# Kernel optimization log

Hardware: AMD Instinct MI355X
Metric: run time of the kernel (lower is better)

The kernel has to match this reference:

```python
import jax, jax.numpy as jnp
import numpy as np

POOL = 14
NUM_ROIS = 512
H, W, C = 200, 200, 1024


def setup_inputs() -> dict:
    key = jax.random.key(0)
    k1, k2, k3, k4, k5 = jax.random.split(key, 5)
    img = jax.random.normal(k1, (1, H, W, C), dtype=jnp.float32)
    # valid boxes: x + w <= W, y + h <= H, w,h >= 8
    x = jax.random.randint(k2, (1, NUM_ROIS), 0, W // 2)
    y = jax.random.randint(k3, (1, NUM_ROIS), 0, H // 2)
    w = jax.random.randint(k4, (1, NUM_ROIS), 8, W // 2)
    h = jax.random.randint(k5, (1, NUM_ROIS), 8, H // 2)
    rois = jnp.stack([x, y, w, h], axis=-1).astype(jnp.int32)  # [1, R, 4]
    return {"img": img, "rois": rois}


def _roi_resize(fm, box):
    # fm: [H, W, C]; box: [4] int32 (x, y, w, h)
    x, y, w, h = box[0], box[1], box[2], box[3]
    # TF1 tf.image.resize_images bilinear, align_corners=False (asymmetric):
    # src = dst * (in_size / out_size), taps floored + clamped to crop extent.
    sy = jnp.arange(POOL, dtype=jnp.float32) * (h.astype(jnp.float32) / POOL)
    sx = jnp.arange(POOL, dtype=jnp.float32) * (w.astype(jnp.float32) / POOL)
    y0 = jnp.floor(sy).astype(jnp.int32)
    x0 = jnp.floor(sx).astype(jnp.int32)
    y0c = jnp.clip(y0, 0, h - 1)
    y1c = jnp.clip(y0 + 1, 0, h - 1)
    x0c = jnp.clip(x0, 0, w - 1)
    x1c = jnp.clip(x0 + 1, 0, w - 1)
    wy = (sy - y0.astype(jnp.float32))[:, None, None]  # [P,1,1]
    wx = (sx - x0.astype(jnp.float32))[None, :, None]  # [1,P,1]
    iy0, iy1 = y + y0c, y + y1c  # absolute row indices
    ix0, ix1 = x + x0c, x + x1c  # absolute col indices
    g00 = fm[iy0[:, None], ix0[None, :]]  # [P,P,C]
    g01 = fm[iy0[:, None], ix1[None, :]]
    g10 = fm[iy1[:, None], ix0[None, :]]
    g11 = fm[iy1[:, None], ix1[None, :]]
    top = g00 + (g01 - g00) * wx
    bot = g10 + (g11 - g10) * wx
    return top + (bot - top) * wy


def reference(img, rois):
    fm = img[0]  # [H, W, C]
    out = jax.vmap(lambda b: _roi_resize(fm, b))(rois[0])  # [R, P, P, C]
    return out[None]  # [1, R, P, P, C]
```

## Files before the change

kernel.cpp:

```cpp
#include <hip/hip_runtime.h>

#define POOL 14
#define NUM_ROIS 512
#define IMG_H 200
#define IMG_W 200
#define IMG_C 1024
#define NUM_XCD 8
#define ROIS_PER_XCD (NUM_ROIS / NUM_XCD)
#define ITEMS_PER_XCD (ROIS_PER_XCD * POOL)
#define XBINS 8
#define NBINS (IMG_H * XBINS)
#define BINS_PER_THREAD 7

typedef float v4f __attribute__((ext_vector_type(4)));

__device__ __forceinline__ int item_key(const int* __restrict__ rois,
                                        int xcd, int i, int* out_code) {
    const int roi_in = i / POOL;
    const int py     = i - roi_in * POOL;
    const int r      = xcd * ROIS_PER_XCD + roi_in;
    const int4 box   = ((const int4*)rois)[r];
    const float stepy = (float)box.w / (float)POOL;
    const float sy    = (float)py * stepy;
    const int y0  = (int)floorf(sy);
    const int y0c = min(max(y0, 0), box.w - 1);
    const int row = box.y + y0c;
    *out_code = (r << 4) | py;
    return row * XBINS + (box.x >> 5);
}

__global__ __launch_bounds__(256) void order_kernel(
    const int* __restrict__ rois, int* __restrict__ perm) {
    const int xcd = blockIdx.x;
    const int tid = threadIdx.x;
    __shared__ int hist[NBINS];
    __shared__ int cnt[NBINS];
    __shared__ int partial[256];

    for (int k = tid; k < NBINS; k += 256) { hist[k] = 0; cnt[k] = 0; }
    __syncthreads();

    for (int i = tid; i < ITEMS_PER_XCD; i += 256) {
        int code;
        atomicAdd(&hist[item_key(rois, xcd, i, &code)], 1);
    }
    __syncthreads();

    const int b0 = tid * BINS_PER_THREAD;
    int lsum[BINS_PER_THREAD];
    int local = 0;
    for (int j = 0; j < BINS_PER_THREAD; ++j) {
        const int k = b0 + j;
        lsum[j] = local;
        if (k < NBINS) local += hist[k];
    }
    partial[tid] = local;
    __syncthreads();
    for (int off = 1; off < 256; off <<= 1) {
        const int add = (tid >= off) ? partial[tid - off] : 0;
        __syncthreads();
        partial[tid] += add;
        __syncthreads();
    }
    const int chunk_excl = partial[tid] - local;
    for (int j = 0; j < BINS_PER_THREAD; ++j) {
        const int k = b0 + j;
        if (k < NBINS) hist[k] = chunk_excl + lsum[j];
    }
    __syncthreads();

    for (int i = tid; i < ITEMS_PER_XCD; i += 256) {
        int code;
        const int key = item_key(rois, xcd, i, &code);
        const int pos = hist[key] + atomicAdd(&cnt[key], 1);
        perm[xcd * ITEMS_PER_XCD + pos] = code;
    }
}

__global__ __launch_bounds__(256) void roi_row_kernel(
    const float* __restrict__ img,
    const int*   __restrict__ rois,
    const int*   __restrict__ perm,
    float*       __restrict__ out)
{
    const int b = blockIdx.x;
    int r, py;
    if (perm) {
        const int code = perm[(b & (NUM_XCD - 1)) * ITEMS_PER_XCD + (b >> 3)];
        r  = code >> 4;
        py = code & 15;
    } else {
        const int xcd = b & (NUM_XCD - 1);
        const int s   = b >> 3;
        const int roi_in = s / POOL;
        py = s - roi_in * POOL;
        r  = xcd * ROIS_PER_XCD + roi_in;
    }

    const int4 box = ((const int4*)rois)[r];
    const int bx = box.x, by = box.y, bw = box.z, bh = box.w;

    const float stepy = (float)bh / (float)POOL;
    const float stepx = (float)bw / (float)POOL;

    const float sy = (float)py * stepy;
    const int   y0 = (int)floorf(sy);
    const float wy = sy - (float)y0;
    const int y0c = min(max(y0, 0), bh - 1);
    const int y1c = min(max(y0 + 1, 0), bh - 1);

    const float* __restrict__ row0 = img + (size_t)(by + y0c) * IMG_W * IMG_C;
    const float* __restrict__ row1 = img + (size_t)(by + y1c) * IMG_W * IMG_C;

    const int c = threadIdx.x * 4;
    float* __restrict__ orow =
        out + ((size_t)r * (POOL * POOL) + (size_t)py * POOL) * IMG_C + c;

#pragma unroll
    for (int px = 0; px < POOL; ++px) {
        const float sx = (float)px * stepx;
        const int   x0 = (int)floorf(sx);
        const float wx = sx - (float)x0;
        const int x0c = min(max(x0, 0), bw - 1);
        const int x1c = min(max(x0 + 1, 0), bw - 1);
        const int ix0 = bx + x0c;
        const int ix1 = bx + x1c;

        const v4f g00 = *(const v4f*)(row0 + (size_t)ix0 * IMG_C + c);
        const v4f g01 = *(const v4f*)(row0 + (size_t)ix1 * IMG_C + c);
        const v4f g10 = *(const v4f*)(row1 + (size_t)ix0 * IMG_C + c);
        const v4f g11 = *(const v4f*)(row1 + (size_t)ix1 * IMG_C + c);

        const v4f top = g00 + (g01 - g00) * wx;
        const v4f bot = g10 + (g11 - g10) * wx;
        const v4f res = top + (bot - top) * wy;

        __builtin_nontemporal_store(res, (v4f*)(orow + (size_t)px * IMG_C));
    }
}

extern "C" void kernel_launch(void* const* d_in, const int* in_sizes, int n_in,
                              void* d_out, int out_size, void* d_ws, size_t ws_size,
                              hipStream_t stream) {
    const float* img  = (const float*)d_in[0];
    const int*   rois = (const int*)d_in[1];
    float*       out  = (float*)d_out;

    int* perm = nullptr;
    if (d_ws && ws_size >= (size_t)(NUM_XCD * ITEMS_PER_XCD) * sizeof(int)) {
        perm = (int*)d_ws;
        order_kernel<<<NUM_XCD, 256, 0, stream>>>(rois, perm);
    }
    roi_row_kernel<<<NUM_ROIS * POOL, 256, 0, stream>>>(img, rois, perm, out);
}
```

Before: 576.5 us.

## Sort all ROI rows globally and deal sorted chunks round-robin across XCDs

The order kernel now sorts all 7168 (roi, row) items in one 1024-thread block by image row and x-bin, instead of sorting each XCD's fixed subset separately. The row kernel maps blocks so that each XCD takes consecutive 112-item chunks of the global sorted order in round-robin. Rows with nearby source pixels then run close together in time on the same XCD, which is meant to raise L2 hit rate for the gathered image rows. The cost is a single-block serial sort with a longer prefix scan, and spatial locality is now spread across all XCDs instead of being confined to one XCD's ROIs.

```diff
diff --git a/kernel.cpp b/kernel.cpp
--- a/kernel.cpp
+++ b/kernel.cpp
@@ -2,26 +2,26 @@
 
 #define POOL 14
 #define NUM_ROIS 512
+#define NUM_ITEMS (NUM_ROIS * POOL)
 #define IMG_H 200
 #define IMG_W 200
 #define IMG_C 1024
 #define NUM_XCD 8
-#define ROIS_PER_XCD (NUM_ROIS / NUM_XCD)
-#define ITEMS_PER_XCD (ROIS_PER_XCD * POOL)
 #define XBINS 8
 #define NBINS (IMG_H * XBINS)
-#define BINS_PER_THREAD 7
+#define CHUNK 112
+#define SORT_THREADS 1024
+#define BINS_PER_THREAD 2
 
 typedef float v4f __attribute__((ext_vector_type(4)));
 
 __device__ __forceinline__ int item_key(const int* __restrict__ rois,
-                                        int xcd, int i, int* out_code) {
-    const int roi_in = i / POOL;
-    const int py     = i - roi_in * POOL;
-    const int r      = xcd * ROIS_PER_XCD + roi_in;
-    const int4 box   = ((const int4*)rois)[r];
+                                        int i, int* out_code) {
+    const int r  = i / POOL;
+    const int py = i - r * POOL;
+    const int4 box = ((const int4*)rois)[r];
     const float stepy = (float)box.w / (float)POOL;
-    const float sy    = (float)py * stepy;
+    const float sy = (float)py * stepy;
     const int y0  = (int)floorf(sy);
     const int y0c = min(max(y0, 0), box.w - 1);
     const int row = box.y + y0c;
@@ -29,20 +29,19 @@
     return row * XBINS + (box.x >> 5);
 }
 
-__global__ __launch_bounds__(256) void order_kernel(
+__global__ __launch_bounds__(SORT_THREADS) void order_kernel(
     const int* __restrict__ rois, int* __restrict__ perm) {
-    const int xcd = blockIdx.x;
     const int tid = threadIdx.x;
     __shared__ int hist[NBINS];
     __shared__ int cnt[NBINS];
-    __shared__ int partial[256];
+    __shared__ int partial[SORT_THREADS];
 
-    for (int k = tid; k < NBINS; k += 256) { hist[k] = 0; cnt[k] = 0; }
+    for (int k = tid; k < NBINS; k += SORT_THREADS) { hist[k] = 0; cnt[k] = 0; }
     __syncthreads();
 
-    for (int i = tid; i < ITEMS_PER_XCD; i += 256) {
+    for (int i = tid; i < NUM_ITEMS; i += SORT_THREADS) {
         int code;
-        atomicAdd(&hist[item_key(rois, xcd, i, &code)], 1);
+        atomicAdd(&hist[item_key(rois, i, &code)], 1);
     }
     __syncthreads();
 
@@ -56,7 +55,7 @@
     }
     partial[tid] = local;
     __syncthreads();
-    for (int off = 1; off < 256; off <<= 1) {
+    for (int off = 1; off < SORT_THREADS; off <<= 1) {
         const int add = (tid >= off) ? partial[tid - off] : 0;
         __syncthreads();
         partial[tid] += add;
@@ -69,11 +68,11 @@
     }
     __syncthreads();
 
-    for (int i = tid; i < ITEMS_PER_XCD; i += 256) {
+    for (int i = tid; i < NUM_ITEMS; i += SORT_THREADS) {
         int code;
-        const int key = item_key(rois, xcd, i, &code);
+        const int key = item_key(rois, i, &code);
         const int pos = hist[key] + atomicAdd(&cnt[key], 1);
-        perm[xcd * ITEMS_PER_XCD + pos] = code;
+        perm[pos] = code;
     }
 }
 
@@ -86,15 +85,17 @@
     const int b = blockIdx.x;
     int r, py;
     if (perm) {
-        const int code = perm[(b & (NUM_XCD - 1)) * ITEMS_PER_XCD + (b >> 3)];
+        const int xcd = b & (NUM_XCD - 1);
+        const int t   = b >> 3;
+        const int cl  = t / CHUNK;
+        const int j   = t - cl * CHUNK;
+        const int pos = (xcd + NUM_XCD * cl) * CHUNK + j;
+        const int code = perm[pos];
         r  = code >> 4;
         py = code & 15;
     } else {
-        const int xcd = b & (NUM_XCD - 1);
-        const int s   = b >> 3;
-        const int roi_in = s / POOL;
-        py = s - roi_in * POOL;
-        r  = xcd * ROIS_PER_XCD + roi_in;
+        r  = b / POOL;
+        py = b - r * POOL;
     }
 
     const int4 box = ((const int4*)rois)[r];
@@ -147,9 +148,9 @@
     float*       out  = (float*)d_out;
 
     int* perm = nullptr;
-    if (d_ws && ws_size >= (size_t)(NUM_XCD * ITEMS_PER_XCD) * sizeof(int)) {
+    if (d_ws && ws_size >= (size_t)NUM_ITEMS * sizeof(int)) {
         perm = (int*)d_ws;
-        order_kernel<<<NUM_XCD, 256, 0, stream>>>(rois, perm);
+        order_kernel<<<1, SORT_THREADS, 0, stream>>>(rois, perm);
     }
-    roi_row_kernel<<<NUM_ROIS * POOL, 256, 0, stream>>>(img, rois, perm, out);
+    roi_row_kernel<<<NUM_ITEMS, 256, 0, stream>>>(img, rois, perm, out);
 }
```

After: 580.8 us. About the same (+0.7%).
